# Kernel tuning notes

Measured on AMD Instinct MI355X. Metric: run time of the kernel, lower is better.

Reference implementation:

```python
import jax, jax.numpy as jnp
import numpy as np

FIELD_SIZE = 39
FEATURE_SIZE = 100000
EMB = 10
BATCH = 2048

# Faithful to the original loop bounds: i in [0, F-2), j in [i+1, F-2)
# i.e. pairs (i, j) with i < j <= FIELD_SIZE - 2 (the last field is skipped
# in the pairwise term due to the original code's range(field_size - 1)).
_pairs = [(i, j) for i in range(FIELD_SIZE - 1) for j in range(i + 1, FIELD_SIZE - 1)]
_I = np.array([p[0] for p in _pairs], dtype=np.int32)  # [P] = [703]
_J = np.array([p[1] for p in _pairs], dtype=np.int32)


def setup_inputs() -> dict:
    key = jax.random.key(0)
    k1, k2, k3, k4 = jax.random.split(key, 4)
    idxs = jax.random.randint(k1, (BATCH, FIELD_SIZE), 0, FEATURE_SIZE)
    vals = jax.random.uniform(k2, (BATCH, FIELD_SIZE), dtype=jnp.float32)
    # stacked field-aware embedding tables: emb_tables[f] == self.emb[f].weight
    emb_tables = jax.random.normal(k3, (FIELD_SIZE, FEATURE_SIZE, EMB), dtype=jnp.float32) * 0.01
    w1 = jax.random.normal(k4, (FEATURE_SIZE, 1), dtype=jnp.float32) * 0.01
    return {"idxs": idxs, "vals": vals, "emb_tables": emb_tables, "w1": w1}


def reference(idxs, vals, emb_tables, w1):
    # first order: sum_f w1[idxs[b,f]] * vals[b,f]
    first = jnp.sum(w1[idxs].squeeze(-1) * vals, axis=1)  # [B]

    i_idx = jnp.asarray(_I)  # [P]
    j_idx = jnp.asarray(_J)  # [P]
    # ffm_second_order_embs[i][:, j] == emb_tables[i, idxs[:, j]] * vals[:, j, None]
    # Only gather the (field, column) entries the pairwise loop actually uses.
    a = emb_tables[i_idx[None, :], idxs[:, j_idx]] * vals[:, j_idx, None]  # [B,P,E]
    b = emb_tables[j_idx[None, :], idxs[:, i_idx]] * vals[:, i_idx, None]  # [B,P,E]
    second = jnp.sum(a * b, axis=(1, 2))  # cat over pairs then sum dim=1 == sum over P and E

    return jax.nn.sigmoid(first + second)  # [B]
```

## Files before the change

### kernel.cpp

```cpp
#include <hip/hip_runtime.h>
#include <math.h>

#define FIELD  39
#define NPF    38
#define NPAIRS 703
#define FEAT   100000
#define EMB    10

__global__ __launch_bounds__(256) void ffm_kernel(
    const int*   __restrict__ idxs,
    const float* __restrict__ vals,
    const float* __restrict__ emb,
    const float* __restrict__ w1,
    float*       __restrict__ out)
{
    const int b = blockIdx.x;
    const int t = threadIdx.x;

    __shared__ int   s_idx[FIELD];
    __shared__ float s_val[FIELD];
    if (t < FIELD) {
        s_idx[t] = idxs[b * FIELD + t];
        s_val[t] = vals[b * FIELD + t];
    }
    __syncthreads();

    float acc = 0.f;
    if (t < FIELD) acc = w1[s_idx[t]] * s_val[t];

    for (int p = t; p < NPAIRS; p += 256) {
        int i = 0, rem = p;
        while (rem >= NPF - 1 - i) { rem -= NPF - 1 - i; ++i; }
        const int j = i + 1 + rem;

        const float2* ea = (const float2*)(emb + ((size_t)i * FEAT + s_idx[j]) * EMB);
        const float2* eb = (const float2*)(emb + ((size_t)j * FEAT + s_idx[i]) * EMB);
        float s = 0.f;
        #pragma unroll
        for (int e = 0; e < 5; ++e) {
            const float2 x = ea[e];
            const float2 y = eb[e];
            s += x.x * y.x + x.y * y.y;
        }
        acc += s * s_val[i] * s_val[j];
    }

    #pragma unroll
    for (int off = 32; off > 0; off >>= 1)
        acc += __shfl_down(acc, off, 64);

    __shared__ float wsum[4];
    if ((t & 63) == 0) wsum[t >> 6] = acc;
    __syncthreads();
    if (t == 0) {
        const float tot = wsum[0] + wsum[1] + wsum[2] + wsum[3];
        out[b] = 1.f / (1.f + expf(-tot));
    }
}

extern "C" void kernel_launch(void* const* d_in, const int* in_sizes, int n_in,
                              void* d_out, int out_size, void* d_ws, size_t ws_size,
                              hipStream_t stream) {
    const int*   idxs = (const int*)  d_in[0];
    const float* vals = (const float*)d_in[1];
    const float* emb  = (const float*)d_in[2];
    const float* w1   = (const float*)d_in[3];
    float*       out  = (float*)d_out;

    ffm_kernel<<<out_size, 256, 0, stream>>>(idxs, vals, emb, w1, out);
}
```

Before: 250.3 us.

## Hoist all pair loads up front with aligned 16-byte vector reads and closed-form decode

```diff
diff --git a/kernel.cpp b/kernel.cpp
--- a/kernel.cpp
+++ b/kernel.cpp
@@ -6,6 +6,24 @@
 #define NPAIRS 703
 #define FEAT   100000
 #define EMB    10
+
+typedef float f4 __attribute__((ext_vector_type(4)));
+
+#define ELT(Q, e) ((e) < 4 ? (Q)[0][(e)] : (e) < 8 ? (Q)[1][(e)-4] : (Q)[2][(e)-8])
+
+__device__ __forceinline__ void decode_pair(int p, int& i_out, int& j_out) {
+    const float disc = 5625.0f - 8.0f * (float)p;
+    int i = (int)((75.0f - sqrtf(disc)) * 0.5f);
+    int off = (i * (75 - i)) >> 1;
+    if (p < off) {
+        --i; off = (i * (75 - i)) >> 1;
+    } else {
+        const int off1 = ((i + 1) * (74 - i)) >> 1;
+        if (p >= off1) { ++i; off = off1; }
+    }
+    i_out = i;
+    j_out = i + 1 + (p - off);
+}
 
 __global__ __launch_bounds__(256) void ffm_kernel(
     const int*   __restrict__ idxs,
@@ -25,24 +43,48 @@
     }
     __syncthreads();
 
-    float acc = 0.f;
-    if (t < FIELD) acc = w1[s_idx[t]] * s_val[t];
+    float acc = (t < FIELD) ? w1[s_idx[t]] * s_val[t] : 0.f;
 
-    for (int p = t; p < NPAIRS; p += 256) {
-        int i = 0, rem = p;
-        while (rem >= NPF - 1 - i) { rem -= NPF - 1 - i; ++i; }
-        const int j = i + 1 + rem;
+    bool  valid[3];
+    int   sha[3], shb[3];
+    float vv[3];
+    const f4* pa[3];
+    const f4* pb[3];
 
-        const float2* ea = (const float2*)(emb + ((size_t)i * FEAT + s_idx[j]) * EMB);
-        const float2* eb = (const float2*)(emb + ((size_t)j * FEAT + s_idx[i]) * EMB);
+    #pragma unroll
+    for (int k = 0; k < 3; ++k) {
+        int p = t + (k << 8);
+        valid[k] = (p < NPAIRS);
+        p = valid[k] ? p : (NPAIRS - 1);
+        int i, j;
+        decode_pair(p, i, j);
+        vv[k] = s_val[i] * s_val[j];
+
+        const size_t byteA = ((size_t)i * FEAT + (size_t)s_idx[j]) * (EMB * 4);
+        const size_t byteB = ((size_t)j * FEAT + (size_t)s_idx[i]) * (EMB * 4);
+        sha[k] = (int)(byteA & 8) >> 2;
+        shb[k] = (int)(byteB & 8) >> 2;
+        pa[k] = (const f4*)((const char*)emb + (byteA & ~(size_t)15));
+        pb[k] = (const f4*)((const char*)emb + (byteB & ~(size_t)15));
+    }
+
+    f4 A[3][3], B[3][3];
+    #pragma unroll
+    for (int k = 0; k < 3; ++k) {
+        A[k][0] = pa[k][0]; A[k][1] = pa[k][1]; A[k][2] = pa[k][2];
+        B[k][0] = pb[k][0]; B[k][1] = pb[k][1]; B[k][2] = pb[k][2];
+    }
+
+    #pragma unroll
+    for (int k = 0; k < 3; ++k) {
         float s = 0.f;
         #pragma unroll
-        for (int e = 0; e < 5; ++e) {
-            const float2 x = ea[e];
-            const float2 y = eb[e];
-            s += x.x * y.x + x.y * y.y;
+        for (int e = 0; e < EMB; ++e) {
+            const float ae = sha[k] ? ELT(A[k], e + 2) : ELT(A[k], e);
+            const float be = shb[k] ? ELT(B[k], e + 2) : ELT(B[k], e);
+            s += ae * be;
         }
-        acc += s * s_val[i] * s_val[j];
+        acc += valid[k] ? s * vv[k] : 0.f;
     }
 
     #pragma unroll
```

Measured after the change: 255.6 us. 1.02x slower.
